# Performance work log

Measured on AMD Instinct MI355X. Metric: run time of the kernel, lower is better.

The kernel has to match this reference:

```python
import jax, jax.numpy as jnp
import numpy as np

NC, M, D = 4, 512, 64
COMMITMENT_COST = 0.25


def setup_inputs() -> dict:
    key = jax.random.key(0)
    k1, k2 = jax.random.split(key)
    N = 65536
    x = jax.random.normal(k1, (N, NC * D), dtype=jnp.float32)
    # original init: uniform(-1/m, 1/m); randn*small keeps comparable scale
    embedding = jax.random.normal(k2, (NC, M, D), dtype=jnp.float32) * (1.0 / M)
    mask = jnp.ones((N, NC), dtype=jnp.float32)
    return {"x": x, "embedding": embedding, "mask": mask}


def reference(x, embedding, mask):
    nc, m, d = embedding.shape
    x_flat = x.reshape(-1, nc, d)                      # (N, nc, d)
    xd = jax.lax.stop_gradient(x_flat)                 # detached copy

    # squared-distance search expressed as a GEMM (same math as sum((x-e)^2)):
    x2 = jnp.sum(xd * xd, axis=-1)[:, :, None]
    e2 = jnp.sum(embedding * embedding, axis=-1)[None, :, :]
    xe = jnp.einsum('ncd,cmd->ncm', xd, embedding)
    distances = x2 - 2.0 * xe + e2

    indices = jnp.argmin(distances, axis=-1)           # (N, nc) int
    # gather nearest code vectors: (N, nc, d)
    quantized = embedding[jnp.arange(nc)[None, :], indices]
    quantized = quantized * mask[..., None]

    codebook_loss = jnp.mean((jax.lax.stop_gradient(x_flat) - quantized) ** 2)
    e_latent_loss = jnp.mean((x_flat - jax.lax.stop_gradient(quantized)) ** 2)
    commitment_loss = COMMITMENT_COST * e_latent_loss

    # straight-through estimator
    quantized_st = x_flat + jax.lax.stop_gradient(quantized - x_flat)
    quantized_st = quantized_st.reshape(x.shape)

    # perplexity via per-codebook histogram (avoids N x nc x m one-hot)
    counts = jax.vmap(lambda idx: jnp.bincount(idx, length=m))(indices.T)  # (nc, m)
    avg_probs = counts.astype(x.dtype) / x_flat.shape[0]
    perplexity = jnp.exp(-jnp.sum(avg_probs * jnp.log(avg_probs + 1e-10)))

    return (quantized_st, commitment_loss, codebook_loss, perplexity, indices)
```

## Files before the change

kernel.cpp:

```cpp
#include <hip/hip_runtime.h>
#include <math.h>
#include <float.h>

#define NTOK 65536
#define NCB  4
#define MCODE 512
#define DIM  64

#define QST_SIZE (NTOK * NCB * DIM)
#define IDX_OFF  (QST_SIZE + 3)

#define TOK_TILE  256
#define XS_STRIDE 68

#define WS_EH 0
#define WS_EL 262144
#define WS_D0 524288
#define WS_CNT 532480
#define WS_LOSS 540672

typedef _Float16 half8 __attribute__((ext_vector_type(8)));
typedef float floatx4 __attribute__((ext_vector_type(4)));

__global__ __launch_bounds__(256) void prep_kernel(const float* __restrict__ emb,
                                                   _Float16* __restrict__ eh,
                                                   _Float16* __restrict__ el,
                                                   float* __restrict__ d0,
                                                   int* __restrict__ counts,
                                                   float* __restrict__ lossSum) {
    int row = blockIdx.x * 256 + threadIdx.x;
    if (row >= NCB * MCODE) return;
    const float* src = emb + (size_t)row * DIM;
    _Float16* ph = eh + (size_t)row * DIM;
    _Float16* pl = el + (size_t)row * DIM;
    float s = 0.f;
#pragma unroll
    for (int j = 0; j < DIM / 8; ++j) {
        half8 h, l;
#pragma unroll
        for (int t = 0; t < 8; ++t) {
            float e = src[j * 8 + t];
            s += e * e;
            float f = e * 512.0f;
            _Float16 hi = (_Float16)f;
            float r = f - (float)hi;
            h[t] = hi;
            l[t] = (_Float16)r;
        }
        *(half8*)(ph + j * 8) = h;
        *(half8*)(pl + j * 8) = l;
    }
    d0[row] = 512.0f * s;
    counts[row] = 0;
    if (row == 0) *lossSum = 0.f;
}

__global__ __launch_bounds__(256) void vq_main(const float* __restrict__ x,
                                               const float* __restrict__ emb,
                                               const float* __restrict__ mask,
                                               const _Float16* __restrict__ eh,
                                               const _Float16* __restrict__ el,
                                               const float* __restrict__ d0,
                                               int* __restrict__ counts,
                                               float* __restrict__ lossSum,
                                               float* __restrict__ outQ,
                                               float* __restrict__ outIdx) {
    __shared__ float Xs[TOK_TILE * XS_STRIDE];
    __shared__ int   Is[TOK_TILE];
    __shared__ float wls[4];

    const int tid  = threadIdx.x;
    const int c    = blockIdx.y;
    const int n0tk = blockIdx.x * TOK_TILE;
    const int lane = tid & 63;
    const int w    = tid >> 6;
    const int col  = lane & 15;
    const int quad = lane >> 4;

#pragma unroll
    for (int i = 0; i < 16; ++i) {
        int q = tid + i * 256;
        int tok = q >> 4, d4 = q & 15;
        float4 v = *(const float4*)(x + (size_t)(n0tk + tok) * (NCB * DIM) + c * DIM + d4 * 4);
        *(float4*)(Xs + tok * XS_STRIDE + d4 * 4) = v;
    }
    __syncthreads();

    half8 Ahi[4][2], Alo[4][2];
#pragma unroll
    for (int s = 0; s < 4; ++s) {
        const float* xr = Xs + (w * 64 + s * 16 + col) * XS_STRIDE;
#pragma unroll
        for (int ks = 0; ks < 2; ++ks) {
            const float* p = xr + ks * 32 + quad * 8;
            half8 h, l;
#pragma unroll
            for (int t = 0; t < 8; ++t) {
                float f = p[t];
                _Float16 hi = (_Float16)f;
                float r = f - (float)hi;
                h[t] = hi;
                l[t] = (_Float16)r;
            }
            Ahi[s][ks] = h;
            Alo[s][ks] = l;
        }
    }

    float minv[4][4];
    int   mini[4][4];
#pragma unroll
    for (int s = 0; s < 4; ++s)
#pragma unroll
        for (int r = 0; r < 4; ++r) { minv[s][r] = FLT_MAX; mini[s][r] = 0; }

    const _Float16* ehc = eh + (size_t)c * MCODE * DIM;
    const _Float16* elc = el + (size_t)c * MCODE * DIM;
    const float*    d0c = d0 + c * MCODE;

#pragma unroll 2
    for (int nt = 0; nt < 32; ++nt) {
        const int nbase = nt * 16;
        const int n = nbase + col;
        const _Float16* bh = ehc + (size_t)n * DIM + quad * 8;
        const _Float16* bl = elc + (size_t)n * DIM + quad * 8;
        half8 Bh0 = *(const half8*)(bh);
        half8 Bh1 = *(const half8*)(bh + 32);
        half8 Bl0 = *(const half8*)(bl);
        half8 Bl1 = *(const half8*)(bl + 32);
        float d0v = d0c[n];

#pragma unroll
        for (int s = 0; s < 4; ++s) {
            floatx4 acc = {0.f, 0.f, 0.f, 0.f};
            acc = __builtin_amdgcn_mfma_f32_16x16x32_f16(Ahi[s][0], Bh0, acc, 0, 0, 0);
            acc = __builtin_amdgcn_mfma_f32_16x16x32_f16(Ahi[s][1], Bh1, acc, 0, 0, 0);
            acc = __builtin_amdgcn_mfma_f32_16x16x32_f16(Alo[s][0], Bh0, acc, 0, 0, 0);
            acc = __builtin_amdgcn_mfma_f32_16x16x32_f16(Alo[s][1], Bh1, acc, 0, 0, 0);
            acc = __builtin_amdgcn_mfma_f32_16x16x32_f16(Ahi[s][0], Bl0, acc, 0, 0, 0);
            acc = __builtin_amdgcn_mfma_f32_16x16x32_f16(Ahi[s][1], Bl1, acc, 0, 0, 0);
#pragma unroll
            for (int r = 0; r < 4; ++r) {
                float dv = fmaf(-2.f, acc[r], d0v);
                if (dv < minv[s][r]) { minv[s][r] = dv; mini[s][r] = n; }
            }
        }
    }

#pragma unroll
    for (int off = 1; off < 16; off <<= 1) {
#pragma unroll
        for (int s = 0; s < 4; ++s)
#pragma unroll
            for (int r = 0; r < 4; ++r) {
                float ov = __shfl_xor(minv[s][r], off);
                int   oi = __shfl_xor(mini[s][r], off);
                if (ov < minv[s][r] || (ov == minv[s][r] && oi < mini[s][r])) {
                    minv[s][r] = ov; mini[s][r] = oi;
                }
            }
    }
    if (col == 0) {
#pragma unroll
        for (int s = 0; s < 4; ++s)
#pragma unroll
            for (int r = 0; r < 4; ++r)
                Is[w * 64 + s * 16 + quad * 4 + r] = mini[s][r];
    }
    __syncthreads();

    {
        int idx = Is[tid];
        atomicAdd(&counts[c * MCODE + idx], 1);
        outIdx[(size_t)(n0tk + tid) * NCB + c] = (float)idx;
    }

    float lloss = 0.f;
#pragma unroll
    for (int i = 0; i < 16; ++i) {
        int q = tid + i * 256;
        int tok = q >> 4, d4 = q & 15;
        int idx = Is[tok];
        float mv = mask[(size_t)(n0tk + tok) * NCB + c];
        float4 e4 = *(const float4*)(emb + ((size_t)c * MCODE + idx) * DIM + d4 * 4);
        float4 x4 = *(const float4*)(Xs + tok * XS_STRIDE + d4 * 4);
        float qx = e4.x * mv, qy = e4.y * mv, qz = e4.z * mv, qw = e4.w * mv;
        float4 o;
        o.x = x4.x + (qx - x4.x);
        o.y = x4.y + (qy - x4.y);
        o.z = x4.z + (qz - x4.z);
        o.w = x4.w + (qw - x4.w);
        *(float4*)(outQ + (size_t)(n0tk + tok) * (NCB * DIM) + c * DIM + d4 * 4) = o;
        float dx = x4.x - qx, dy = x4.y - qy, dz = x4.z - qz, dw = x4.w - qw;
        lloss += dx * dx + dy * dy + dz * dz + dw * dw;
    }
#pragma unroll
    for (int off = 32; off > 0; off >>= 1) lloss += __shfl_xor(lloss, off);
    if ((tid & 63) == 0) wls[tid >> 6] = lloss;
    __syncthreads();
    if (tid == 0) {
        float s = wls[0] + wls[1] + wls[2] + wls[3];
        atomicAdd(lossSum, s);
    }
}

__global__ __launch_bounds__(256) void finalize_kernel(const int* __restrict__ counts,
                                                       const float* __restrict__ lossSum,
                                                       float* __restrict__ out) {
    __shared__ float wls[4];
    int tid = threadIdx.x;
    float s = 0.f;
#pragma unroll
    for (int i = 0; i < 8; ++i) {
        int j = tid + i * 256;
        float p = (float)counts[j] * (1.0f / 65536.0f);
        s += p * logf(p + 1e-10f);
    }
#pragma unroll
    for (int off = 32; off > 0; off >>= 1) s += __shfl_xor(s, off);
    if ((tid & 63) == 0) wls[tid >> 6] = s;
    __syncthreads();
    if (tid == 0) {
        float tot = wls[0] + wls[1] + wls[2] + wls[3];
        float L = *lossSum * (1.0f / (float)QST_SIZE);
        out[QST_SIZE + 0] = 0.25f * L;
        out[QST_SIZE + 1] = L;
        out[QST_SIZE + 2] = expf(-tot);
    }
}

extern "C" void kernel_launch(void* const* d_in, const int* in_sizes, int n_in,
                              void* d_out, int out_size, void* d_ws, size_t ws_size,
                              hipStream_t stream) {
    const float* x    = (const float*)d_in[0];
    const float* emb  = (const float*)d_in[1];
    const float* mask = (const float*)d_in[2];
    float* out = (float*)d_out;

    _Float16* eh   = (_Float16*)((char*)d_ws + WS_EH);
    _Float16* el   = (_Float16*)((char*)d_ws + WS_EL);
    float* d0      = (float*)((char*)d_ws + WS_D0);
    int*   counts  = (int*)((char*)d_ws + WS_CNT);
    float* lossSum = (float*)((char*)d_ws + WS_LOSS);

    prep_kernel<<<dim3(8), dim3(256), 0, stream>>>(emb, eh, el, d0, counts, lossSum);
    vq_main<<<dim3(NTOK / TOK_TILE, NCB), dim3(256), 0, stream>>>(
        x, emb, mask, eh, el, d0, counts, lossSum, out, out + IDX_OFF);
    finalize_kernel<<<dim3(1), dim3(256), 0, stream>>>(counts, lossSum, out);
}
```

Measured before the change: 221.4 us.

## Switch distance GEMM to 32x32 MFMA with pre-swizzled codebook and bias-initialized accumulator

The main kernel moves from 16x16x32 to 32x32x16 MFMA and swaps operand roles, so codes become the A operand and tokens the B operand loaded straight from global memory. The prep kernel writes the split-fp16 codebook in an MFMA-friendly swizzled layout and stores -||e||^2/2 scaled, which is used as the accumulator's initial value so the argmin becomes an argmax with no per-element FMA. The token tile shrinks to 128 and the shared-memory X staging is removed, with x re-read from global in the epilogue. This trades shared-memory traffic and reduction shuffles for a second global read of x and a different occupancy profile.

```diff
diff --git a/kernel.cpp b/kernel.cpp
--- a/kernel.cpp
+++ b/kernel.cpp
@@ -10,8 +10,7 @@
 #define QST_SIZE (NTOK * NCB * DIM)
 #define IDX_OFF  (QST_SIZE + 3)
 
-#define TOK_TILE  256
-#define XS_STRIDE 68
+#define TOK_TILE  128
 
 #define WS_EH 0
 #define WS_EL 262144
@@ -20,37 +19,44 @@
 #define WS_LOSS 540672
 
 typedef _Float16 half8 __attribute__((ext_vector_type(8)));
-typedef float floatx4 __attribute__((ext_vector_type(4)));
+typedef float floatx16 __attribute__((ext_vector_type(16)));
 
 __global__ __launch_bounds__(256) void prep_kernel(const float* __restrict__ emb,
-                                                   _Float16* __restrict__ eh,
-                                                   _Float16* __restrict__ el,
-                                                   float* __restrict__ d0,
+                                                   _Float16* __restrict__ ehf,
+                                                   _Float16* __restrict__ elf,
+                                                   float* __restrict__ d0p,
                                                    int* __restrict__ counts,
                                                    float* __restrict__ lossSum) {
     int row = blockIdx.x * 256 + threadIdx.x;
     if (row >= NCB * MCODE) return;
+    const int c   = row >> 9;
+    const int n   = row & 511;
+    const int nt  = n >> 5;
+    const int r5  = n & 31;
     const float* src = emb + (size_t)row * DIM;
-    _Float16* ph = eh + (size_t)row * DIM;
-    _Float16* pl = el + (size_t)row * DIM;
+
     float s = 0.f;
 #pragma unroll
-    for (int j = 0; j < DIM / 8; ++j) {
-        half8 h, l;
-#pragma unroll
-        for (int t = 0; t < 8; ++t) {
-            float e = src[j * 8 + t];
-            s += e * e;
-            float f = e * 512.0f;
-            _Float16 hi = (_Float16)f;
-            float r = f - (float)hi;
-            h[t] = hi;
-            l[t] = (_Float16)r;
+    for (int ch = 0; ch < 4; ++ch) {
+#pragma unroll
+        for (int h = 0; h < 2; ++h) {
+            half8 hv, lv;
+#pragma unroll
+            for (int t = 0; t < 8; ++t) {
+                float e = src[ch * 16 + h * 8 + t];
+                s += e * e;
+                float f = e * 512.0f;
+                _Float16 hi = (_Float16)f;
+                float r = f - (float)hi;
+                hv[t] = hi;
+                lv[t] = (_Float16)r;
+            }
+            size_t off = ((size_t)((c * 16 + nt) * 4 + ch)) * 512 + (h * 32 + r5) * 8;
+            *(half8*)(ehf + off) = hv;
+            *(half8*)(elf + off) = lv;
         }
-        *(half8*)(ph + j * 8) = h;
-        *(half8*)(pl + j * 8) = l;
-    }
-    d0[row] = 512.0f * s;
+    }
+    d0p[row] = -256.0f * s;
     counts[row] = 0;
     if (row == 0) *lossSum = 0.f;
 }
@@ -58,14 +64,13 @@
 __global__ __launch_bounds__(256) void vq_main(const float* __restrict__ x,
                                                const float* __restrict__ emb,
                                                const float* __restrict__ mask,
-                                               const _Float16* __restrict__ eh,
-                                               const _Float16* __restrict__ el,
-                                               const float* __restrict__ d0,
+                                               const _Float16* __restrict__ ehf,
+                                               const _Float16* __restrict__ elf,
+                                               const float* __restrict__ d0p,
                                                int* __restrict__ counts,
                                                float* __restrict__ lossSum,
                                                float* __restrict__ outQ,
                                                float* __restrict__ outIdx) {
-    __shared__ float Xs[TOK_TILE * XS_STRIDE];
     __shared__ int   Is[TOK_TILE];
     __shared__ float wls[4];
 
@@ -74,116 +79,105 @@
     const int n0tk = blockIdx.x * TOK_TILE;
     const int lane = tid & 63;
     const int w    = tid >> 6;
-    const int col  = lane & 15;
-    const int quad = lane >> 4;
-
-#pragma unroll
-    for (int i = 0; i < 16; ++i) {
-        int q = tid + i * 256;
-        int tok = q >> 4, d4 = q & 15;
-        float4 v = *(const float4*)(x + (size_t)(n0tk + tok) * (NCB * DIM) + c * DIM + d4 * 4);
-        *(float4*)(Xs + tok * XS_STRIDE + d4 * 4) = v;
+    const int l31  = lane & 31;
+    const int hi   = lane >> 5;
+    const int hi4  = hi * 4;
+
+    half8 Bh[4], Bl[4];
+    {
+        const float* xr = x + (size_t)(n0tk + w * 32 + l31) * (NCB * DIM) + c * DIM + hi * 8;
+#pragma unroll
+        for (int ch = 0; ch < 4; ++ch) {
+            float fv[8];
+            *(float4*)(fv)     = *(const float4*)(xr + ch * 16);
+            *(float4*)(fv + 4) = *(const float4*)(xr + ch * 16 + 4);
+            half8 h8, l8;
+#pragma unroll
+            for (int t = 0; t < 8; ++t) {
+                float f = fv[t];
+                _Float16 hh = (_Float16)f;
+                h8[t] = hh;
+                l8[t] = (_Float16)(f - (float)hh);
+            }
+            Bh[ch] = h8;
+            Bl[ch] = l8;
+        }
+    }
+
+    const _Float16* Ah_base = ehf + (size_t)c * (16 * 4 * 512) + (size_t)lane * 8;
+    const _Float16* Al_base = elf + (size_t)c * (16 * 4 * 512) + (size_t)lane * 8;
+    const float*    d0c     = d0p + c * MCODE;
+
+    float maxv = -FLT_MAX;
+    int   maxn = 0;
+
+    for (int nt = 0; nt < 16; ++nt) {
+        const _Float16* pah = Ah_base + (size_t)nt * 2048;
+        const _Float16* pal = Al_base + (size_t)nt * 2048;
+        half8 Ah0 = *(const half8*)(pah);
+        half8 Ah1 = *(const half8*)(pah + 512);
+        half8 Ah2 = *(const half8*)(pah + 1024);
+        half8 Ah3 = *(const half8*)(pah + 1536);
+        half8 Al0 = *(const half8*)(pal);
+        half8 Al1 = *(const half8*)(pal + 512);
+        half8 Al2 = *(const half8*)(pal + 1024);
+        half8 Al3 = *(const half8*)(pal + 1536);
+
+        const float* dpt = d0c + nt * 32 + hi4;
+        float4 d40 = *(const float4*)(dpt);
+        float4 d41 = *(const float4*)(dpt + 8);
+        float4 d42 = *(const float4*)(dpt + 16);
+        float4 d43 = *(const float4*)(dpt + 24);
+        floatx16 acc;
+        acc[0]  = d40.x; acc[1]  = d40.y; acc[2]  = d40.z; acc[3]  = d40.w;
+        acc[4]  = d41.x; acc[5]  = d41.y; acc[6]  = d41.z; acc[7]  = d41.w;
+        acc[8]  = d42.x; acc[9]  = d42.y; acc[10] = d42.z; acc[11] = d42.w;
+        acc[12] = d43.x; acc[13] = d43.y; acc[14] = d43.z; acc[15] = d43.w;
+
+        acc = __builtin_amdgcn_mfma_f32_32x32x16_f16(Ah0, Bh[0], acc, 0, 0, 0);
+        acc = __builtin_amdgcn_mfma_f32_32x32x16_f16(Al0, Bh[0], acc, 0, 0, 0);
+        acc = __builtin_amdgcn_mfma_f32_32x32x16_f16(Ah0, Bl[0], acc, 0, 0, 0);
+        acc = __builtin_amdgcn_mfma_f32_32x32x16_f16(Ah1, Bh[1], acc, 0, 0, 0);
+        acc = __builtin_amdgcn_mfma_f32_32x32x16_f16(Al1, Bh[1], acc, 0, 0, 0);
+        acc = __builtin_amdgcn_mfma_f32_32x32x16_f16(Ah1, Bl[1], acc, 0, 0, 0);
+        acc = __builtin_amdgcn_mfma_f32_32x32x16_f16(Ah2, Bh[2], acc, 0, 0, 0);
+        acc = __builtin_amdgcn_mfma_f32_32x32x16_f16(Al2, Bh[2], acc, 0, 0, 0);
+        acc = __builtin_amdgcn_mfma_f32_32x32x16_f16(Ah2, Bl[2], acc, 0, 0, 0);
+        acc = __builtin_amdgcn_mfma_f32_32x32x16_f16(Ah3, Bh[3], acc, 0, 0, 0);
+        acc = __builtin_amdgcn_mfma_f32_32x32x16_f16(Al3, Bh[3], acc, 0, 0, 0);
+        acc = __builtin_amdgcn_mfma_f32_32x32x16_f16(Ah3, Bl[3], acc, 0, 0, 0);
+
+        const int nbase = nt * 32 + hi4;
+#pragma unroll
+        for (int r = 0; r < 16; ++r) {
+            float m = acc[r];
+            int   n = nbase + ((r & 3) + 8 * (r >> 2));
+            if (m > maxv) { maxv = m; maxn = n; }
+        }
+    }
+
+    {
+        float ov = __shfl_xor(maxv, 32);
+        int   on = __shfl_xor(maxn, 32);
+        if (ov > maxv || (ov == maxv && on < maxn)) { maxv = ov; maxn = on; }
+    }
+
+    if (hi == 0) {
+        Is[w * 32 + l31] = maxn;
+        atomicAdd(&counts[c * MCODE + maxn], 1);
+        outIdx[(size_t)(n0tk + w * 32 + l31) * NCB + c] = (float)maxn;
     }
     __syncthreads();
 
-    half8 Ahi[4][2], Alo[4][2];
-#pragma unroll
-    for (int s = 0; s < 4; ++s) {
-        const float* xr = Xs + (w * 64 + s * 16 + col) * XS_STRIDE;
-#pragma unroll
-        for (int ks = 0; ks < 2; ++ks) {
-            const float* p = xr + ks * 32 + quad * 8;
-            half8 h, l;
-#pragma unroll
-            for (int t = 0; t < 8; ++t) {
-                float f = p[t];
-                _Float16 hi = (_Float16)f;
-                float r = f - (float)hi;
-                h[t] = hi;
-                l[t] = (_Float16)r;
-            }
-            Ahi[s][ks] = h;
-            Alo[s][ks] = l;
-        }
-    }
-
-    float minv[4][4];
-    int   mini[4][4];
-#pragma unroll
-    for (int s = 0; s < 4; ++s)
-#pragma unroll
-        for (int r = 0; r < 4; ++r) { minv[s][r] = FLT_MAX; mini[s][r] = 0; }
-
-    const _Float16* ehc = eh + (size_t)c * MCODE * DIM;
-    const _Float16* elc = el + (size_t)c * MCODE * DIM;
-    const float*    d0c = d0 + c * MCODE;
-
-#pragma unroll 2
-    for (int nt = 0; nt < 32; ++nt) {
-        const int nbase = nt * 16;
-        const int n = nbase + col;
-        const _Float16* bh = ehc + (size_t)n * DIM + quad * 8;
-        const _Float16* bl = elc + (size_t)n * DIM + quad * 8;
-        half8 Bh0 = *(const half8*)(bh);
-        half8 Bh1 = *(const half8*)(bh + 32);
-        half8 Bl0 = *(const half8*)(bl);
-        half8 Bl1 = *(const half8*)(bl + 32);
-        float d0v = d0c[n];
-
-#pragma unroll
-        for (int s = 0; s < 4; ++s) {
-            floatx4 acc = {0.f, 0.f, 0.f, 0.f};
-            acc = __builtin_amdgcn_mfma_f32_16x16x32_f16(Ahi[s][0], Bh0, acc, 0, 0, 0);
-            acc = __builtin_amdgcn_mfma_f32_16x16x32_f16(Ahi[s][1], Bh1, acc, 0, 0, 0);
-            acc = __builtin_amdgcn_mfma_f32_16x16x32_f16(Alo[s][0], Bh0, acc, 0, 0, 0);
-            acc = __builtin_amdgcn_mfma_f32_16x16x32_f16(Alo[s][1], Bh1, acc, 0, 0, 0);
-            acc = __builtin_amdgcn_mfma_f32_16x16x32_f16(Ahi[s][0], Bl0, acc, 0, 0, 0);
-            acc = __builtin_amdgcn_mfma_f32_16x16x32_f16(Ahi[s][1], Bl1, acc, 0, 0, 0);
-#pragma unroll
-            for (int r = 0; r < 4; ++r) {
-                float dv = fmaf(-2.f, acc[r], d0v);
-                if (dv < minv[s][r]) { minv[s][r] = dv; mini[s][r] = n; }
-            }
-        }
-    }
-
-#pragma unroll
-    for (int off = 1; off < 16; off <<= 1) {
-#pragma unroll
-        for (int s = 0; s < 4; ++s)
-#pragma unroll
-            for (int r = 0; r < 4; ++r) {
-                float ov = __shfl_xor(minv[s][r], off);
-                int   oi = __shfl_xor(mini[s][r], off);
-                if (ov < minv[s][r] || (ov == minv[s][r] && oi < mini[s][r])) {
-                    minv[s][r] = ov; mini[s][r] = oi;
-                }
-            }
-    }
-    if (col == 0) {
-#pragma unroll
-        for (int s = 0; s < 4; ++s)
-#pragma unroll
-            for (int r = 0; r < 4; ++r)
-                Is[w * 64 + s * 16 + quad * 4 + r] = mini[s][r];
-    }
-    __syncthreads();
-
-    {
-        int idx = Is[tid];
-        atomicAdd(&counts[c * MCODE + idx], 1);
-        outIdx[(size_t)(n0tk + tid) * NCB + c] = (float)idx;
-    }
-
     float lloss = 0.f;
 #pragma unroll
-    for (int i = 0; i < 16; ++i) {
+    for (int i = 0; i < 8; ++i) {
         int q = tid + i * 256;
         int tok = q >> 4, d4 = q & 15;
         int idx = Is[tok];
         float mv = mask[(size_t)(n0tk + tok) * NCB + c];
         float4 e4 = *(const float4*)(emb + ((size_t)c * MCODE + idx) * DIM + d4 * 4);
-        float4 x4 = *(const float4*)(Xs + tok * XS_STRIDE + d4 * 4);
+        float4 x4 = *(const float4*)(x + (size_t)(n0tk + tok) * (NCB * DIM) + c * DIM + d4 * 4);
         float qx = e4.x * mv, qy = e4.y * mv, qz = e4.z * mv, qw = e4.w * mv;
         float4 o;
         o.x = x4.x + (qx - x4.x);
@@ -237,14 +231,14 @@
     const float* mask = (const float*)d_in[2];
     float* out = (float*)d_out;
 
-    _Float16* eh   = (_Float16*)((char*)d_ws + WS_EH);
-    _Float16* el   = (_Float16*)((char*)d_ws + WS_EL);
-    float* d0      = (float*)((char*)d_ws + WS_D0);
+    _Float16* ehf  = (_Float16*)((char*)d_ws + WS_EH);
+    _Float16* elf  = (_Float16*)((char*)d_ws + WS_EL);
+    float* d0p     = (float*)((char*)d_ws + WS_D0);
     int*   counts  = (int*)((char*)d_ws + WS_CNT);
     float* lossSum = (float*)((char*)d_ws + WS_LOSS);
 
-    prep_kernel<<<dim3(8), dim3(256), 0, stream>>>(emb, eh, el, d0, counts, lossSum);
+    prep_kernel<<<dim3(8), dim3(256), 0, stream>>>(emb, ehf, elf, d0p, counts, lossSum);
     vq_main<<<dim3(NTOK / TOK_TILE, NCB), dim3(256), 0, stream>>>(
-        x, emb, mask, eh, el, d0, counts, lossSum, out, out + IDX_OFF);
+        x, emb, mask, ehf, elf, d0p, counts, lossSum, out, out + IDX_OFF);
     finalize_kernel<<<dim3(1), dim3(256), 0, stream>>>(counts, lossSum, out);
 }
```

Measured after the change: 211.3 us. 4.6% less time.
